# Optimization experiments

Hardware: AMD Instinct MI355X
Metric: run time of the kernel (lower is better)

The kernel has to match this reference:

```python
import jax, jax.numpy as jnp
import numpy as np

D_MODEL = 1024
NUM_HEADS = 16
ROPE_THETA = 10000.0


def _rope(v, pos, theta=ROPE_THETA):
    # v: [B, S, D] (full d_model, as in the original module), pos: [B, S] int
    d = v.shape[-1]
    inv_freq = theta ** (-jnp.arange(0, d, 2, dtype=jnp.float32) / d)  # [D/2]
    ang = pos.astype(jnp.float32)[..., None] * inv_freq  # [B, S, D/2]
    cos, sin = jnp.cos(ang), jnp.sin(ang)
    x1, x2 = v[..., ::2], v[..., 1::2]
    r1 = x1 * cos - x2 * sin
    r2 = x1 * sin + x2 * cos
    return jnp.stack([r1, r2], axis=-1).reshape(v.shape)


def setup_inputs() -> dict:
    key = jax.random.key(0)
    ks = jax.random.split(key, 6)
    B, S, D = 2, 2048, D_MODEL
    std = np.sqrt(2.0 / (D + D)).astype(np.float32)
    x = jax.random.normal(ks[0], (B, S, D), dtype=jnp.float32)
    token_positions = jnp.sort(jax.random.randint(ks[1], (B, S), 0, S), axis=-1).astype(jnp.int32)
    wq = jax.random.normal(ks[2], (D, D), dtype=jnp.float32) * std
    wk = jax.random.normal(ks[3], (D, D), dtype=jnp.float32) * std
    wv = jax.random.normal(ks[4], (D, D), dtype=jnp.float32) * std
    wo = jax.random.normal(ks[5], (D, D), dtype=jnp.float32) * std
    return {"x": x, "token_positions": token_positions, "wq": wq, "wk": wk, "wv": wv, "wo": wo}


def reference(x, token_positions, wq, wk, wv, wo):
    B, S, D = x.shape
    H = NUM_HEADS
    dk = D // H
    # Projections (nn.functional.linear: x @ W^T)
    q = x @ wq.T
    k = x @ wk.T
    v = x @ wv.T
    # In the original, Q/K are reshaped to heads and back before RoPE -> identity;
    # RoPE is applied over the FULL d_model dimension.
    q = _rope(q, token_positions)
    k = _rope(k, token_positions)
    # Split heads
    q = q.reshape(B, S, H, dk)
    k = k.reshape(B, S, H, dk)
    v = v.reshape(B, S, H, dk)
    scores = jnp.einsum('bqhd,bkhd->bhqk', q, k) / jnp.sqrt(jnp.asarray(dk, x.dtype))
    causal = jnp.tril(jnp.ones((S, S), dtype=bool))  # True where allowed
    scores = jnp.where(causal[None, None], scores, -jnp.inf)
    attn = jax.nn.softmax(scores, axis=-1)
    out = jnp.einsum('bhqk,bkhd->bqhd', attn, v).reshape(B, S, D)
    return out @ wo.T
```

## Files before the change

### kernel.cpp

```cpp
#include <hip/hip_runtime.h>
#include <hip/hip_bf16.h>
#include <math.h>

typedef __attribute__((ext_vector_type(8))) short bf16x8;
typedef __attribute__((ext_vector_type(4))) short short4x;
typedef __attribute__((ext_vector_type(4))) float f32x4;
typedef __attribute__((ext_vector_type(8))) float f32x8;

#define D_MODEL 1024
#define NHEADS  16
#define DK      64
#define BATCH   2
#define SEQ     2048

static __device__ __forceinline__ short f2bf(float f) {
    unsigned u = __builtin_bit_cast(unsigned, f);
    u = u + 0x7FFFu + ((u >> 16) & 1u);
    return (short)(u >> 16);
}
static __device__ __forceinline__ short f2bf_fast(float f) {
    return (short)((__builtin_bit_cast(unsigned, f) + 0x8000u) >> 16);
}
static __device__ __forceinline__ float bf2f(short s) {
    return __builtin_bit_cast(float, ((unsigned)(unsigned short)s) << 16);
}

typedef __attribute__((address_space(3))) unsigned int lds_uint;
typedef __attribute__((address_space(1))) const unsigned int glob_uint;
static __device__ __forceinline__ void gl2lds16(const short* g, short* l) {
    __builtin_amdgcn_global_load_lds((glob_uint*)g, (lds_uint*)l, 16, 0, 0);
}

#define NX8 ((BATCH * SEQ * D_MODEL) / 8)
#define NW8 ((D_MODEL * D_MODEL) / 8)
__global__ void cvt_all_kernel(const void* __restrict__ x,  const void* __restrict__ wq,
                               const void* __restrict__ wk, const void* __restrict__ wv,
                               const void* __restrict__ wo,
                               __hip_bfloat16* __restrict__ xb,  __hip_bfloat16* __restrict__ wqb,
                               __hip_bfloat16* __restrict__ wkb, __hip_bfloat16* __restrict__ wvb,
                               __hip_bfloat16* __restrict__ wob,
                               int* __restrict__ dtf)
{
    __shared__ int sflag;
    if (threadIdx.x < 64) {
        const unsigned w = ((const unsigned*)x)[threadIdx.x];
        const unsigned e = (w >> 7) & 0xFFu;
        const bool weird = (e >= 0x88u) || (e <= 0x5Fu);
        const unsigned long long m = __ballot(weird);
        if (threadIdx.x == 0) {
            const int f = (__popcll(m) >= 16) ? 1 : 0;
            sflag = f;
            if (blockIdx.x == 0) *dtf = f;
        }
    }
    __syncthreads();

    const int i = blockIdx.x * blockDim.x + threadIdx.x;
    if (i >= NX8 + 4 * NW8) return;
    const void* src; __hip_bfloat16* dst; int off;
    if (i < NX8) { src = x; dst = xb; off = i; }
    else {
        const int j = i - NX8, seg = j >> 17; off = j & (NW8 - 1);
        switch (seg) {
            case 0: src = wq; dst = wqb; break;
            case 1: src = wk; dst = wkb; break;
            case 2: src = wv; dst = wvb; break;
            default: src = wo; dst = wob; break;
        }
    }
    if (sflag) {
        const f32x8 v = ((const f32x8*)src)[off];
        bf16x8 r;
#pragma unroll
        for (int j = 0; j < 8; ++j) r[j] = f2bf(v[j]);
        ((bf16x8*)dst)[off] = r;
    } else {
        ((bf16x8*)dst)[off] = ((const bf16x8*)src)[off];
    }
}

static __device__ __forceinline__ void gemm128_main(
    const short* __restrict__ A, const short* __restrict__ B,
    int K, int bm, int bn, f32x4 (&acc)[4][4], short* lds)
{
    const int tid  = threadIdx.x;
    const int lane = tid & 63;
    const int wave = tid >> 6;
    const int l16  = lane & 15;
    const int quad = lane >> 4;

    const int srow = lane >> 2;
    const int scg  = (lane & 3) ^ ((lane >> 3) & 3);
    const short* ag = A + (size_t)(bm + wave * 32 + srow) * K + scg * 8;
    const short* bg = B + (size_t)(bn + wave * 32 + srow) * K + scg * 8;
    const int dst = wave * 1024 + lane * 8;

    const int mrow = (wave >> 1) * 64;
    const int nrow = (wave & 1) * 64;
    const int ph   = ((quad ^ ((l16 >> 1) & 3))) * 8;

    auto stage = [&](int k0, int buf) {
        short* ad = lds + buf * 4096 + dst;
        short* bd = lds + 8192 + buf * 4096 + dst;
        gl2lds16(ag + k0, ad);
        gl2lds16(ag + k0 + (size_t)16 * K, ad + 512);
        gl2lds16(bg + k0, bd);
        gl2lds16(bg + k0 + (size_t)16 * K, bd + 512);
    };

    stage(0, 0);
    for (int k0 = 0, t = 0; k0 < K; k0 += 32, ++t) {
        __asm__ volatile("s_waitcnt vmcnt(0)" ::: "memory");
        __syncthreads();
        if (k0 + 32 < K) stage(k0 + 32, (t + 1) & 1);

        const short* Ab = lds + (t & 1) * 4096;
        const short* Bb = lds + 8192 + (t & 1) * 4096;
        bf16x8 a[4], b[4];
#pragma unroll
        for (int x = 0; x < 4; ++x)
            a[x] = *(const bf16x8*)(Ab + (mrow + x * 16 + l16) * 32 + ph);
#pragma unroll
        for (int y = 0; y < 4; ++y)
            b[y] = *(const bf16x8*)(Bb + (nrow + y * 16 + l16) * 32 + ph);
#pragma unroll
        for (int x = 0; x < 4; ++x)
#pragma unroll
            for (int y = 0; y < 4; ++y)
                acc[x][y] = __builtin_amdgcn_mfma_f32_16x16x32_bf16(
                    a[x], b[y], acc[x][y], 0, 0, 0);
    }
}

__global__ __launch_bounds__(256) void gemm_qkv_kernel(
    const __hip_bfloat16* __restrict__ xb,
    const __hip_bfloat16* __restrict__ wqb,
    const __hip_bfloat16* __restrict__ wkb,
    const __hip_bfloat16* __restrict__ wvb,
    const int* __restrict__ pos,
    __hip_bfloat16* __restrict__ Qb,
    __hip_bfloat16* __restrict__ Kb,
    __hip_bfloat16* __restrict__ Vt)
{
    __shared__ alignas(16) short lds[16384];
    const int wsel = blockIdx.x >> 3;
    const int bn   = (blockIdx.x & 7) * 128;
    const int bm   = blockIdx.y * 128;
    const short* W = (const short*)(wsel == 0 ? wqb : (wsel == 1 ? wkb : wvb));

    f32x4 acc[4][4];
#pragma unroll
    for (int x = 0; x < 4; ++x)
#pragma unroll
        for (int y = 0; y < 4; ++y) acc[x][y] = (f32x4){0.f, 0.f, 0.f, 0.f};

    gemm128_main((const short*)xb, W, D_MODEL, bm, bn, acc, lds);

    const int lane = threadIdx.x & 63;
    const int wave = threadIdx.x >> 6;
    const int l16  = lane & 15;
    const int quad = lane >> 4;

    if (wsel == 2) {
#pragma unroll
        for (int x = 0; x < 4; ++x)
#pragma unroll
            for (int y = 0; y < 4; ++y)
#pragma unroll
                for (int r = 0; r < 4; ++r) {
                    const int row = bm + (wave >> 1) * 64 + x * 16 + quad * 4 + r;
                    const int col = bn + (wave & 1) * 64 + y * 16 + l16;
                    const int hh = col >> 6, dcol = col & 63;
                    const int bb = row >> 11, ss = row & (SEQ - 1);
                    Vt[(((size_t)bb * NHEADS + hh) * DK + dcol) * SEQ + ss] =
                        __float2bfloat16(acc[x][y][r]);
                }
        return;
    }

    __hip_bfloat16* Crm = (wsel == 1) ? Kb : Qb;
    const float qscale = (wsel == 0) ? 0.125f : 1.0f;
#pragma unroll
    for (int x = 0; x < 4; ++x)
#pragma unroll
        for (int r = 0; r < 4; ++r) {
            const int row = bm + (wave >> 1) * 64 + x * 16 + quad * 4 + r;
            const float p = (float)pos[row];
#pragma unroll
            for (int y = 0; y < 4; ++y) {
                const int col = bn + (wave & 1) * 64 + y * 16 + l16;
                const float inv = exp2f((float)(col >> 1) * -0.02595256257f);
                const float ang = p * inv;
                const float c = __cosf(ang), s = __sinf(ang);
                const float v  = acc[x][y][r];
                const float pv = __shfl_xor(v, 1);
                const float vr = v * c + pv * ((l16 & 1) ? s : -s);
                Crm[(size_t)row * D_MODEL + col] = __float2bfloat16(vr * qscale);
            }
        }
}

__global__ __launch_bounds__(256) void gemm_out_kernel(
    const __hip_bfloat16* __restrict__ AO,
    const __hip_bfloat16* __restrict__ wob,
    void* __restrict__ C, const int* __restrict__ dtf)
{
    __shared__ alignas(16) short lds[2][6144];
    const int tid  = threadIdx.x;
    const int lane = tid & 63;
    const int wave = tid >> 6;
    const int l16  = lane & 15;
    const int quad = lane >> 4;
    const int bn = blockIdx.x * 128;
    const int bm = blockIdx.y * 64;
    const bool c32 = (*dtf) != 0;
    const int K = D_MODEL;

    const int srow = lane >> 2;
    const int scg  = (lane & 3) ^ ((lane >> 3) & 3);
    const short* Ap = (const short*)AO;
    const short* Bp = (const short*)wob;
    const short* ag = Ap + (size_t)(bm + wave * 16 + srow) * K + scg * 8;
    const short* bg = Bp + (size_t)(bn + wave * 32 + srow) * K + scg * 8;

    const int nrow = wave * 32;
    const int ph   = ((quad ^ ((l16 >> 1) & 3))) * 8;

    f32x4 acc[4][2];
#pragma unroll
    for (int x = 0; x < 4; ++x)
#pragma unroll
        for (int y = 0; y < 2; ++y) acc[x][y] = (f32x4){0.f, 0.f, 0.f, 0.f};

    auto stage = [&](int k0, int buf) {
        gl2lds16(ag + k0, &lds[buf][wave * 512 + lane * 8]);
        gl2lds16(bg + k0, &lds[buf][2048 + wave * 1024 + lane * 8]);
        gl2lds16(bg + k0 + (size_t)16 * K, &lds[buf][2048 + wave * 1024 + 512 + lane * 8]);
    };

    stage(0, 0);
    for (int k0 = 0, t = 0; k0 < K; k0 += 32, ++t) {
        __asm__ volatile("s_waitcnt vmcnt(0)" ::: "memory");
        __syncthreads();
        if (k0 + 32 < K) stage(k0 + 32, (t + 1) & 1);

        const short* Ab = &lds[t & 1][0];
        const short* Bb = &lds[t & 1][2048];
        bf16x8 a[4], b[2];
#pragma unroll
        for (int x = 0; x < 4; ++x)
            a[x] = *(const bf16x8*)(Ab + (x * 16 + l16) * 32 + ph);
#pragma unroll
        for (int y = 0; y < 2; ++y)
            b[y] = *(const bf16x8*)(Bb + (nrow + y * 16 + l16) * 32 + ph);
#pragma unroll
        for (int x = 0; x < 4; ++x)
#pragma unroll
            for (int y = 0; y < 2; ++y)
                acc[x][y] = __builtin_amdgcn_mfma_f32_16x16x32_bf16(
                    a[x], b[y], acc[x][y], 0, 0, 0);
    }

#pragma unroll
    for (int x = 0; x < 4; ++x)
#pragma unroll
        for (int y = 0; y < 2; ++y)
#pragma unroll
            for (int r = 0; r < 4; ++r) {
                const int row = bm + x * 16 + quad * 4 + r;
                const int col = bn + nrow + y * 16 + l16;
                const size_t idx = (size_t)row * D_MODEL + col;
                if (c32) ((float*)C)[idx] = acc[x][y][r];
                else     ((__hip_bfloat16*)C)[idx] = __float2bfloat16(acc[x][y][r]);
            }
}

__global__ __launch_bounds__(256, 2) void flash_attn_kernel(
    __hip_bfloat16* QO,
    const __hip_bfloat16* __restrict__ Kt,
    const __hip_bfloat16* __restrict__ Vt)
{
    __shared__ alignas(16) char pool[66560];
    short* k_lds = (short*)pool;
    short* v_lds = (short*)(pool + 32768);

    const int lane = threadIdx.x & 63;
    const int wave = threadIdx.x >> 6;
    const int l16  = lane & 15;
    const int quad = lane >> 4;
    const int qt   = 31 - blockIdx.y;
    const int bh   = blockIdx.x;
    const int b    = bh >> 4;
    const int h    = bh & 15;
    const size_t base  = (size_t)b * SEQ * D_MODEL + h * DK;
    const size_t vbase = (size_t)bh * DK * SEQ;

    const short* Qp = (const short*)QO;
    const short* Kp = (const short*)Kt;
    const short* Vp = (const short*)Vt;

    bf16x8 aq[4][2];
#pragma unroll
    for (int qf = 0; qf < 4; ++qf)
#pragma unroll
        for (int ks = 0; ks < 2; ++ks)
            aq[qf][ks] = *(const bf16x8*)(Qp + base +
                (size_t)(qt * 64 + qf * 16 + l16) * D_MODEL + ks * 32 + quad * 8);

    f32x4 o[4][4];
    float ls[4] = {0.f, 0.f, 0.f, 0.f};
#pragma unroll
    for (int qf = 0; qf < 4; ++qf)
#pragma unroll
        for (int nf = 0; nf < 4; ++nf) o[qf][nf] = (f32x4){0.f, 0.f, 0.f, 0.f};

    const int srow = lane >> 3;
    const int scg  = (lane & 7) ^ srow;
    const short* kg = Kp + ((size_t)b * SEQ + wave * 32 + srow) * D_MODEL + h * DK + scg * 8;
    const int ge = (l16 & 8) | ((l16 & 7) ^ quad);
    const int go = (l16 & 8) | ((l16 & 7) ^ (4 + quad));
    const short* vgA = Vp + vbase + (size_t)(wave * 16 + quad) * SEQ + ge * 8;
    const short* vgB = Vp + vbase + (size_t)(wave * 16 + 4 + quad) * SEQ + go * 8;

    auto stage = [&](int t, int buf) {
        const int kv0 = t * 128;
        short* kd = k_lds + buf * 8192 + (wave * 32) * 64 + lane * 8;
#pragma unroll
        for (int i = 0; i < 4; ++i)
            gl2lds16(kg + (size_t)(kv0 + i * 8) * D_MODEL, kd + i * 8 * 64);
        short* vd = v_lds + buf * 8192 + (wave * 16) * 128 + lane * 8;
        gl2lds16(vgA + kv0,                 vd);
        gl2lds16(vgB + kv0,                 vd + 4 * 128);
        gl2lds16(vgA + (size_t)8 * SEQ + kv0, vd + 8 * 128);
        gl2lds16(vgB + (size_t)8 * SEQ + kv0, vd + 12 * 128);
    };

    auto compute = [&](int buf, int kv0, bool tail) {
        const short* kb = k_lds + buf * 8192;
        const short* vb = v_lds + buf * 8192;
        bf16x8 ak[2][2];
#pragma unroll
        for (int kvf = 0; kvf < 2; ++kvf)
#pragma unroll
            for (int ks = 0; ks < 2; ++ks) {
                const int row = wave * 32 + kvf * 16 + l16;
                const int g = (ks * 4 + quad) ^ (l16 & 7);
                ak[kvf][ks] = *(const bf16x8*)(kb + row * 64 + g * 8);
            }
        f32x4 s[2][4];
        __builtin_amdgcn_s_setprio(1);
#pragma unroll
        for (int kvf = 0; kvf < 2; ++kvf)
#pragma unroll
            for (int qf = 0; qf < 4; ++qf) {
                f32x4 c = (f32x4){0.f, 0.f, 0.f, 0.f};
                c = __builtin_amdgcn_mfma_f32_16x16x32_bf16(ak[kvf][0], aq[qf][0], c, 0, 0, 0);
                c = __builtin_amdgcn_mfma_f32_16x16x32_bf16(ak[kvf][1], aq[qf][1], c, 0, 0, 0);
                s[kvf][qf] = c;
            }
        __builtin_amdgcn_s_setprio(0);

        bf16x8 pa[4];
#pragma unroll
        for (int qf = 0; qf < 4; ++qf) {
            const int qrow = qt * 64 + qf * 16 + l16;
#pragma unroll
            for (int kvf = 0; kvf < 2; ++kvf)
#pragma unroll
                for (int r = 0; r < 4; ++r) {
                    float p = __expf(s[kvf][qf][r]);
                    if (tail && (kv0 + wave * 32 + kvf * 16 + quad * 4 + r > qrow))
                        p = 0.f;
                    ls[qf] += p;
                    pa[qf][kvf * 4 + r] = f2bf_fast(p);
                }
        }

        if (tail) { __asm__ volatile("s_waitcnt vmcnt(0)" ::: "memory"); }
        else      { __asm__ volatile("s_waitcnt vmcnt(8)" ::: "memory"); }
        __builtin_amdgcn_s_barrier();

        bf16x8 bv[4];
#pragma unroll
        for (int nf = 0; nf < 4; ++nf) {
            const int d = nf * 16 + l16;
#pragma unroll
            for (int e = 0; e < 2; ++e) {
                const int g  = wave * 4 + e * 2 + (quad >> 1);
                const int gs = (g & 8) | ((g & 7) ^ (l16 & 7));
                const short4x v4 = *(const short4x*)(vb + d * 128 + gs * 8 + (quad & 1) * 4);
                bv[nf][e * 4 + 0] = v4[0];
                bv[nf][e * 4 + 1] = v4[1];
                bv[nf][e * 4 + 2] = v4[2];
                bv[nf][e * 4 + 3] = v4[3];
            }
        }
        __builtin_amdgcn_s_setprio(1);
#pragma unroll
        for (int qf = 0; qf < 4; ++qf)
#pragma unroll
            for (int nf = 0; nf < 4; ++nf)
                o[qf][nf] = __builtin_amdgcn_mfma_f32_16x16x32_bf16(
                    pa[qf], bv[nf], o[qf][nf], 0, 0, 0);
        __builtin_amdgcn_s_setprio(0);
    };

    const int tmax = qt >> 1;
    stage(0, 0);
    for (int t = 0; t < tmax; ++t) {
        __asm__ volatile("s_waitcnt vmcnt(4)" ::: "memory");
        __syncthreads();
        stage(t + 1, (t + 1) & 1);
        compute(t & 1, t * 128, false);
    }
    __asm__ volatile("s_waitcnt vmcnt(4)" ::: "memory");
    __syncthreads();
    compute(tmax & 1, tmax * 128, true);

#pragma unroll
    for (int qf = 0; qf < 4; ++qf) {
        ls[qf] += __shfl_xor(ls[qf], 16);
        ls[qf] += __shfl_xor(ls[qf], 32);
    }
    __syncthreads();
    float* red = (float*)pool;
    float* lsb = (float*)(pool + 65536);
#pragma unroll
    for (int qf = 0; qf < 4; ++qf)
#pragma unroll
        for (int nf = 0; nf < 4; ++nf)
            *(f32x4*)(red + ((wave * 16 + qf * 4 + nf) * 64 + lane) * 4) = o[qf][nf];
    if (quad == 0)
#pragma unroll
        for (int qf = 0; qf < 4; ++qf) lsb[wave * 64 + qf * 16 + l16] = ls[qf];
    __syncthreads();

    f32x4 lden = (f32x4){0.f, 0.f, 0.f, 0.f};
#pragma unroll
    for (int w = 0; w < 4; ++w)
        lden += *(const f32x4*)(lsb + w * 64 + wave * 16 + quad * 4);
    f32x4 osum[4];
#pragma unroll
    for (int nf = 0; nf < 4; ++nf) {
        f32x4 a = (f32x4){0.f, 0.f, 0.f, 0.f};
#pragma unroll
        for (int w = 0; w < 4; ++w)
            a += *(const f32x4*)(red + ((w * 16 + wave * 4 + nf) * 64 + lane) * 4);
        osum[nf] = a;
    }
    float inv[4];
#pragma unroll
    for (int r = 0; r < 4; ++r) inv[r] = 1.f / fmaxf(lden[r], 1e-20f);
#pragma unroll
    for (int nf = 0; nf < 4; ++nf)
#pragma unroll
        for (int r = 0; r < 4; ++r)
            QO[base + (size_t)(qt * 64 + wave * 16 + quad * 4 + r) * D_MODEL
                    + nf * 16 + l16]
                = __float2bfloat16(osum[nf][r] * inv[r]);
}

extern "C" void kernel_launch(void* const* d_in, const int* in_sizes, int n_in,
                              void* d_out, int out_size, void* d_ws, size_t ws_size,
                              hipStream_t stream)
{
    (void)in_sizes; (void)n_in; (void)out_size; (void)ws_size;

    const void* x  = d_in[0];
    const int*  pos = (const int*)d_in[1];
    const void* wq = d_in[2];
    const void* wk = d_in[3];
    const void* wv = d_in[4];
    const void* wo = d_in[5];

    const int M = BATCH * SEQ;
    const int D = D_MODEL;
    const size_t MD = (size_t)M * D;
    const size_t DD = (size_t)D * D;

    int* dtf = (int*)d_ws;
    __hip_bfloat16* xb  = (__hip_bfloat16*)((char*)d_ws + 256);
    __hip_bfloat16* wqb = xb  + MD;
    __hip_bfloat16* wkb = wqb + DD;
    __hip_bfloat16* wvb = wkb + DD;
    __hip_bfloat16* wob = wvb + DD;
    __hip_bfloat16* Qb  = wob + DD;
    __hip_bfloat16* Vtb = Qb  + MD;
    __hip_bfloat16* Kb  = (__hip_bfloat16*)d_out;

    dim3 blk(256);

    const int ncvt = NX8 + 4 * NW8;
    hipLaunchKernelGGL(cvt_all_kernel, dim3((ncvt + 255) / 256), blk, 0, stream,
                       x, wq, wk, wv, wo, xb, wqb, wkb, wvb, wob, dtf);

    hipLaunchKernelGGL(gemm_qkv_kernel, dim3(24, 32), blk, 0, stream,
                       xb, wqb, wkb, wvb, pos, Qb, Kb, Vtb);

    hipLaunchKernelGGL(flash_attn_kernel, dim3(32, 32), blk, 0, stream,
                       Qb, Kb, Vtb);

    hipLaunchKernelGGL(gemm_out_kernel, dim3(D / 128, M / 64), blk, 0, stream,
                       Qb, wob, d_out, dtf);
}
```

Measured before the change: 172.7 us.

## Triple-buffer LDS staging in QKV and output projection GEMMs

Replaces the double-buffered global-to-LDS pipeline in both projection GEMMs with a three-stage ring that keeps two future K-tiles in flight. Partial vmcnt waits replace the full drain each iteration, so loads overlap MFMA compute more deeply. This costs more shared memory per block, which may reduce occupancy, and adds a second barrier per iteration to protect buffer reuse.

```diff
diff --git a/kernel.cpp b/kernel.cpp
--- a/kernel.cpp
+++ b/kernel.cpp
@@ -99,23 +99,26 @@
     const int nrow = (wave & 1) * 64;
     const int ph   = ((quad ^ ((l16 >> 1) & 3))) * 8;
 
-    auto stage = [&](int k0, int buf) {
-        short* ad = lds + buf * 4096 + dst;
-        short* bd = lds + 8192 + buf * 4096 + dst;
+    auto stage = [&](int t) {
+        const int k0 = t * 32;
+        short* ad = lds + (t % 3) * 8192 + dst;
+        short* bd = ad + 4096;
         gl2lds16(ag + k0, ad);
         gl2lds16(ag + k0 + (size_t)16 * K, ad + 512);
         gl2lds16(bg + k0, bd);
         gl2lds16(bg + k0 + (size_t)16 * K, bd + 512);
     };
 
-    stage(0, 0);
-    for (int k0 = 0, t = 0; k0 < K; k0 += 32, ++t) {
-        __asm__ volatile("s_waitcnt vmcnt(0)" ::: "memory");
-        __syncthreads();
-        if (k0 + 32 < K) stage(k0 + 32, (t + 1) & 1);
-
-        const short* Ab = lds + (t & 1) * 4096;
-        const short* Bb = lds + 8192 + (t & 1) * 4096;
+    const int NT = K / 32;
+    stage(0); stage(1); stage(2);
+    for (int t = 0; t < NT; ++t) {
+        if (t + 2 < NT)      { __asm__ volatile("s_waitcnt vmcnt(8)" ::: "memory"); }
+        else if (t + 1 < NT) { __asm__ volatile("s_waitcnt vmcnt(4)" ::: "memory"); }
+        else                 { __asm__ volatile("s_waitcnt vmcnt(0)" ::: "memory"); }
+        __builtin_amdgcn_s_barrier();
+
+        const short* Ab = lds + (t % 3) * 8192;
+        const short* Bb = Ab + 4096;
         bf16x8 a[4], b[4];
 #pragma unroll
         for (int x = 0; x < 4; ++x)
@@ -129,6 +132,9 @@
             for (int y = 0; y < 4; ++y)
                 acc[x][y] = __builtin_amdgcn_mfma_f32_16x16x32_bf16(
                     a[x], b[y], acc[x][y], 0, 0, 0);
+
+        __builtin_amdgcn_s_barrier();
+        if (t + 3 < NT) stage(t + 3);
     }
 }
 
@@ -142,7 +148,7 @@
     __hip_bfloat16* __restrict__ Kb,
     __hip_bfloat16* __restrict__ Vt)
 {
-    __shared__ alignas(16) short lds[16384];
+    __shared__ alignas(16) short lds[3 * 8192];
     const int wsel = blockIdx.x >> 3;
     const int bn   = (blockIdx.x & 7) * 128;
     const int bm   = blockIdx.y * 128;
@@ -205,7 +211,7 @@
     const __hip_bfloat16* __restrict__ wob,
     void* __restrict__ C, const int* __restrict__ dtf)
 {
-    __shared__ alignas(16) short lds[2][6144];
+    __shared__ alignas(16) short lds[3][6144];
     const int tid  = threadIdx.x;
     const int lane = tid & 63;
     const int wave = tid >> 6;
@@ -232,20 +238,24 @@
 #pragma unroll
         for (int y = 0; y < 2; ++y) acc[x][y] = (f32x4){0.f, 0.f, 0.f, 0.f};
 
-    auto stage = [&](int k0, int buf) {
-        gl2lds16(ag + k0, &lds[buf][wave * 512 + lane * 8]);
-        gl2lds16(bg + k0, &lds[buf][2048 + wave * 1024 + lane * 8]);
-        gl2lds16(bg + k0 + (size_t)16 * K, &lds[buf][2048 + wave * 1024 + 512 + lane * 8]);
+    auto stage = [&](int t) {
+        const int k0 = t * 32;
+        short* base = &lds[t % 3][0];
+        gl2lds16(ag + k0, base + wave * 512 + lane * 8);
+        gl2lds16(bg + k0, base + 2048 + wave * 1024 + lane * 8);
+        gl2lds16(bg + k0 + (size_t)16 * K, base + 2048 + wave * 1024 + 512 + lane * 8);
     };
 
-    stage(0, 0);
-    for (int k0 = 0, t = 0; k0 < K; k0 += 32, ++t) {
-        __asm__ volatile("s_waitcnt vmcnt(0)" ::: "memory");
-        __syncthreads();
-        if (k0 + 32 < K) stage(k0 + 32, (t + 1) & 1);
-
-        const short* Ab = &lds[t & 1][0];
-        const short* Bb = &lds[t & 1][2048];
+    const int NT = K / 32;
+    stage(0); stage(1); stage(2);
+    for (int t = 0; t < NT; ++t) {
+        if (t + 2 < NT)      { __asm__ volatile("s_waitcnt vmcnt(6)" ::: "memory"); }
+        else if (t + 1 < NT) { __asm__ volatile("s_waitcnt vmcnt(3)" ::: "memory"); }
+        else                 { __asm__ volatile("s_waitcnt vmcnt(0)" ::: "memory"); }
+        __builtin_amdgcn_s_barrier();
+
+        const short* Ab = &lds[t % 3][0];
+        const short* Bb = Ab + 2048;
         bf16x8 a[4], b[2];
 #pragma unroll
         for (int x = 0; x < 4; ++x)
@@ -259,6 +269,9 @@
             for (int y = 0; y < 2; ++y)
                 acc[x][y] = __builtin_amdgcn_mfma_f32_16x16x32_bf16(
                     a[x], b[y], acc[x][y], 0, 0, 0);
+
+        __builtin_amdgcn_s_barrier();
+        if (t + 3 < NT) stage(t + 3);
     }
 
 #pragma unroll
```

Measured after the change: 176.6 us. 2.2% more time.
